# Performance work log

Measured on AMD Instinct MI355X. Metric: run time of the kernel, lower is better.

## Reference

```python
import jax, jax.numpy as jnp
import numpy as np

MAX_SHIFT = 15            # sampling_rate // 2 with sampling_rate = 30
NUM_SHIFTS = 2 * MAX_SHIFT + 1


def setup_inputs() -> dict:
    key = jax.random.key(0)
    k1, k2, k3, k4 = jax.random.split(key, 4)
    B, T, P = 128, 16384, 32
    y_pred = jax.random.normal(k1, (B, T), dtype=jnp.float32)
    y_true = jax.random.normal(k2, (B, T), dtype=jnp.float32)
    # theta_s: per-participant latent shift logits (init 1/S in torch; random here)
    theta = jax.random.normal(k3, (P, NUM_SHIFTS), dtype=jnp.float32) * 0.1
    participant_idx = jax.random.randint(k4, (B,), 0, P, dtype=jnp.int32)
    return {"y_pred": y_pred, "y_true": y_true, "theta": theta,
            "participant_idx": participant_idx}


def reference(y_pred, y_true, theta, participant_idx):
    # y_pred, y_true: [B, T]; theta: [P, S]; participant_idx: [B]
    B, T = y_pred.shape
    M = MAX_SHIFT
    S = NUM_SHIFTS
    # Zero-pad both sides; slice start M+shift reproduces the torch pad logic
    # for both negative and positive shifts (out-of-range values are 0).
    padded = jnp.pad(y_true, ((0, 0), (M, M)))              # [B, T+2M]
    idx = jnp.arange(S)[:, None] + jnp.arange(T)[None, :]   # [S, T]
    shifted = padded[:, idx]                                # [B, S, T]
    mse_per_shift = jnp.mean((y_pred[:, None, :] - shifted) ** 2, axis=-1)  # [B, S]
    # training path: participant-wise softmax mixture over shifts
    p_k = jax.nn.softmax(theta[participant_idx], axis=-1)   # [B, S]
    return jnp.mean(jnp.sum(mse_per_shift * p_k, axis=-1))
```

## Files before the change

kernel.cpp:

```cpp
#include <hip/hip_runtime.h>

#define T_LEN 16384
#define B_N   128
#define S_N   31
#define M_SH  15
#define NCHUNK 8
#define TCHUNK (T_LEN / NCHUNK)
#define BLOCK  256
#define VT     8
#define NBLOCKS (B_N * NCHUNK)
#define HALO   16
#define TILE_F4 ((TCHUNK + 2 * HALO) / 4)

__device__ __forceinline__ int swz(int f4) { return f4 ^ ((f4 >> 3) & 7); }

__global__ __launch_bounds__(BLOCK) void talos_main(
    const float* __restrict__ y_pred,
    const float* __restrict__ y_true,
    const float* __restrict__ theta,
    const int* __restrict__ pidx,
    float* __restrict__ partial) {

  __shared__ float tile[TILE_F4 * 4];
  __shared__ float wsh[S_N];
  __shared__ float redL[BLOCK / 64];

  const int bid   = blockIdx.x;
  const int b     = bid / NCHUNK;
  const int chunk = bid % NCHUNK;
  const int t0    = chunk * TCHUNK;
  const int tid   = threadIdx.x;
  const float* yt_b = y_true + b * T_LEN;
  const float* yp_b = y_pred + b * T_LEN;

  for (int f = tid; f < TILE_F4; f += BLOCK) {
    int g = t0 - HALO + f * 4;
    float4 v;
    if (g >= 0 && g + 3 < T_LEN) {
      v = *(const float4*)(yt_b + g);
    } else {
      v.x = (g + 0 >= 0 && g + 0 < T_LEN) ? yt_b[g + 0] : 0.f;
      v.y = (g + 1 >= 0 && g + 1 < T_LEN) ? yt_b[g + 1] : 0.f;
      v.z = (g + 2 >= 0 && g + 2 < T_LEN) ? yt_b[g + 2] : 0.f;
      v.w = (g + 3 >= 0 && g + 3 < T_LEN) ? yt_b[g + 3] : 0.f;
    }
    *(float4*)&tile[swz(f) * 4] = v;
  }

  if (tid < 32) {
    float v = (tid < S_N) ? theta[pidx[b] * S_N + tid] : -1e30f;
    float m = v;
#pragma unroll
    for (int off = 16; off; off >>= 1) m = fmaxf(m, __shfl_xor(m, off, 32));
    float e = (tid < S_N) ? __expf(v - m) : 0.f;
    float s = e;
#pragma unroll
    for (int off = 16; off; off >>= 1) s += __shfl_xor(s, off, 32);
    if (tid < S_N) wsh[tid] = e / s;
  }
  __syncthreads();

  const int lt0 = tid * VT;
  float yp[VT];
  *(float4*)&yp[0] = *(const float4*)(yp_b + t0 + lt0);
  *(float4*)&yp[4] = *(const float4*)(yp_b + t0 + lt0 + 4);

  float win[VT + 2 * HALO];
#pragma unroll
  for (int q = 0; q < (VT + 2 * HALO) / 4; ++q) {
    int f4 = (lt0 >> 2) + q;
    *(float4*)&win[q * 4] = *(const float4*)&tile[swz(f4) * 4];
  }

  float lin[VT];
#pragma unroll
  for (int j = 0; j < VT; ++j) lin[j] = 0.f;
#pragma unroll
  for (int s = 0; s < S_N; ++s) {
    const float ws = wsh[s];
#pragma unroll
    for (int j = 0; j < VT; ++j)
      lin[j] = fmaf(ws, win[j + s + 1], lin[j]);
  }

  float acc = 0.f;
#pragma unroll
  for (int j = 0; j < VT; ++j) {
    acc = fmaf(yp[j], fmaf(-2.f, lin[j], yp[j]), acc);
    float a = win[HALO + j];
    acc = fmaf(a, a, acc);
  }

  if (chunk == 0 && tid < M_SH) {
    float a = yt_b[tid];
    float tw = 0.f;
#pragma unroll
    for (int k = 1; k <= M_SH; ++k) if (k > tid) tw += wsh[k + M_SH];
    acc -= a * a * tw;
  }
  if (chunk == NCHUNK - 1 && tid < M_SH) {
    const int j = tid + 1;
    float z = yt_b[T_LEN - j];
    float tw = 0.f;
#pragma unroll
    for (int k = 1; k <= M_SH; ++k) if (k >= j) tw += wsh[M_SH - k];
    acc -= z * z * tw;
  }

#pragma unroll
  for (int off = 32; off; off >>= 1) acc += __shfl_down(acc, off, 64);
  const int lane = tid & 63, wv = tid >> 6;
  if (lane == 0) redL[wv] = acc;
  __syncthreads();
  if (tid == 0) {
    float P = 0.f;
#pragma unroll
    for (int i = 0; i < BLOCK / 64; ++i) P += redL[i];
    partial[bid] = P;
  }
}

__global__ __launch_bounds__(BLOCK) void talos_tail(
    const float* __restrict__ partial, float* __restrict__ out) {
  __shared__ double redD[BLOCK / 64];
  const int tid = threadIdx.x;
  float4 v = *(const float4*)(partial + tid * 4);
  double a = (double)v.x + (double)v.y + (double)v.z + (double)v.w;
#pragma unroll
  for (int off = 32; off; off >>= 1) a += __shfl_down(a, off, 64);
  const int lane = tid & 63, wv = tid >> 6;
  if (lane == 0) redD[wv] = a;
  __syncthreads();
  if (tid == 0) {
    double tot = 0.0;
#pragma unroll
    for (int i = 0; i < BLOCK / 64; ++i) tot += redD[i];
    out[0] = (float)(tot / ((double)T_LEN * (double)B_N));
  }
}

extern "C" void kernel_launch(void* const* d_in, const int* in_sizes, int n_in,
                              void* d_out, int out_size, void* d_ws, size_t ws_size,
                              hipStream_t stream) {
  const float* y_pred = (const float*)d_in[0];
  const float* y_true = (const float*)d_in[1];
  const float* theta  = (const float*)d_in[2];
  const int*   pidx   = (const int*)d_in[3];
  float* out = (float*)d_out;
  float* partial = (float*)d_ws;

  talos_main<<<NBLOCKS, BLOCK, 0, stream>>>(y_pred, y_true, theta, pidx, partial);
  talos_tail<<<1, BLOCK, 0, stream>>>(partial, out);
}
```

Before: 11.61 us.

## Issue all global loads early with nontemporal hints and shrink tail reduction

Moves the theta and y_pred loads ahead of the shared-memory tile fill so they are in flight together. The tile loop is unrolled into three explicit steps, and the middle step skips bounds checks. Global loads use nontemporal hints, and launch bounds now request 4 blocks per CU. The tail kernel becomes a single wave that sums with shuffles only, removing the LDS round trip and block barrier. The idea is to overlap memory latency and cut sync overhead, but the nontemporal hints may bypass cache reuse of the tile halos shared with neighbouring blocks.

```diff
diff --git a/kernel.cpp b/kernel.cpp
--- a/kernel.cpp
+++ b/kernel.cpp
@@ -12,9 +12,15 @@
 #define HALO   16
 #define TILE_F4 ((TCHUNK + 2 * HALO) / 4)
 
+typedef float fx4 __attribute__((ext_vector_type(4)));
+
 __device__ __forceinline__ int swz(int f4) { return f4 ^ ((f4 >> 3) & 7); }
 
-__global__ __launch_bounds__(BLOCK) void talos_main(
+__device__ __forceinline__ fx4 ntload4(const float* p) {
+  return __builtin_nontemporal_load((const fx4*)p);
+}
+
+__global__ __launch_bounds__(BLOCK, 4) void talos_main(
     const float* __restrict__ y_pred,
     const float* __restrict__ y_true,
     const float* __restrict__ theta,
@@ -33,26 +39,53 @@
   const float* yt_b = y_true + b * T_LEN;
   const float* yp_b = y_pred + b * T_LEN;
 
-  for (int f = tid; f < TILE_F4; f += BLOCK) {
+  float thv = -1e30f;
+  if (tid < S_N) thv = theta[pidx[b] * S_N + tid];
+
+  const int lt0 = tid * VT;
+  float yp[VT];
+  *(fx4*)&yp[0] = ntload4(yp_b + t0 + lt0);
+  *(fx4*)&yp[4] = ntload4(yp_b + t0 + lt0 + 4);
+
+  {
+    int f = tid;
     int g = t0 - HALO + f * 4;
-    float4 v;
+    fx4 v;
     if (g >= 0 && g + 3 < T_LEN) {
-      v = *(const float4*)(yt_b + g);
+      v = ntload4(yt_b + g);
     } else {
       v.x = (g + 0 >= 0 && g + 0 < T_LEN) ? yt_b[g + 0] : 0.f;
       v.y = (g + 1 >= 0 && g + 1 < T_LEN) ? yt_b[g + 1] : 0.f;
       v.z = (g + 2 >= 0 && g + 2 < T_LEN) ? yt_b[g + 2] : 0.f;
       v.w = (g + 3 >= 0 && g + 3 < T_LEN) ? yt_b[g + 3] : 0.f;
     }
-    *(float4*)&tile[swz(f) * 4] = v;
+    *(fx4*)&tile[swz(f) * 4] = v;
+
+    f = tid + BLOCK;
+    g = t0 - HALO + f * 4;
+    v = ntload4(yt_b + g);
+    *(fx4*)&tile[swz(f) * 4] = v;
+
+    if (tid < TILE_F4 - 2 * BLOCK) {
+      f = tid + 2 * BLOCK;
+      g = t0 - HALO + f * 4;
+      if (g + 3 < T_LEN) {
+        v = ntload4(yt_b + g);
+      } else {
+        v.x = (g + 0 < T_LEN) ? yt_b[g + 0] : 0.f;
+        v.y = (g + 1 < T_LEN) ? yt_b[g + 1] : 0.f;
+        v.z = (g + 2 < T_LEN) ? yt_b[g + 2] : 0.f;
+        v.w = (g + 3 < T_LEN) ? yt_b[g + 3] : 0.f;
+      }
+      *(fx4*)&tile[swz(f) * 4] = v;
+    }
   }
 
   if (tid < 32) {
-    float v = (tid < S_N) ? theta[pidx[b] * S_N + tid] : -1e30f;
-    float m = v;
+    float m = thv;
 #pragma unroll
     for (int off = 16; off; off >>= 1) m = fmaxf(m, __shfl_xor(m, off, 32));
-    float e = (tid < S_N) ? __expf(v - m) : 0.f;
+    float e = (tid < S_N) ? __expf(thv - m) : 0.f;
     float s = e;
 #pragma unroll
     for (int off = 16; off; off >>= 1) s += __shfl_xor(s, off, 32);
@@ -60,16 +93,11 @@
   }
   __syncthreads();
 
-  const int lt0 = tid * VT;
-  float yp[VT];
-  *(float4*)&yp[0] = *(const float4*)(yp_b + t0 + lt0);
-  *(float4*)&yp[4] = *(const float4*)(yp_b + t0 + lt0 + 4);
-
   float win[VT + 2 * HALO];
 #pragma unroll
   for (int q = 0; q < (VT + 2 * HALO) / 4; ++q) {
     int f4 = (lt0 >> 2) + q;
-    *(float4*)&win[q * 4] = *(const float4*)&tile[swz(f4) * 4];
+    *(fx4*)&win[q * 4] = *(const fx4*)&tile[swz(f4) * 4];
   }
 
   float lin[VT];
@@ -120,23 +148,19 @@
   }
 }
 
-__global__ __launch_bounds__(BLOCK) void talos_tail(
+__global__ __launch_bounds__(64) void talos_tail(
     const float* __restrict__ partial, float* __restrict__ out) {
-  __shared__ double redD[BLOCK / 64];
   const int tid = threadIdx.x;
-  float4 v = *(const float4*)(partial + tid * 4);
-  double a = (double)v.x + (double)v.y + (double)v.z + (double)v.w;
+  double a = 0.0;
+#pragma unroll
+  for (int q = 0; q < 4; ++q) {
+    fx4 v = *(const fx4*)(partial + (q * 64 + tid) * 4);
+    a += (double)v.x + (double)v.y + (double)v.z + (double)v.w;
+  }
 #pragma unroll
   for (int off = 32; off; off >>= 1) a += __shfl_down(a, off, 64);
-  const int lane = tid & 63, wv = tid >> 6;
-  if (lane == 0) redD[wv] = a;
-  __syncthreads();
-  if (tid == 0) {
-    double tot = 0.0;
-#pragma unroll
-    for (int i = 0; i < BLOCK / 64; ++i) tot += redD[i];
-    out[0] = (float)(tot / ((double)T_LEN * (double)B_N));
-  }
+  if (tid == 0)
+    out[0] = (float)(a / ((double)T_LEN * (double)B_N));
 }
 
 extern "C" void kernel_launch(void* const* d_in, const int* in_sizes, int n_in,
@@ -150,5 +174,5 @@
   float* partial = (float*)d_ws;
 
   talos_main<<<NBLOCKS, BLOCK, 0, stream>>>(y_pred, y_true, theta, pidx, partial);
-  talos_tail<<<1, BLOCK, 0, stream>>>(partial, out);
+  talos_tail<<<1, 64, 0, stream>>>(partial, out);
 }
```

After: 11.52 us. About the same (-0.8%).
